# Kernel optimization log

Hardware: AMD Instinct MI355X
Metric: run time of the kernel (lower is better)

## Reference

```python
import jax, jax.numpy as jnp
import numpy as np

HEADS = 8
EPS = 1e-5


def _layernorm(x, g, b):
    mu = jnp.mean(x, axis=-1, keepdims=True)
    var = jnp.mean(jnp.square(x - mu), axis=-1, keepdims=True)
    return (x - mu) * jax.lax.rsqrt(var + EPS) * g + b


def setup_inputs() -> dict:
    key = jax.random.key(0)
    ks = jax.random.split(key, 10)
    B, S, D = 4, 2048, 256
    d_ff = 2 * D
    s = 0.02
    return {
        "x": jax.random.normal(ks[0], (B, S, D), dtype=jnp.float32),
        "ln1_g": jnp.ones((D,), jnp.float32),
        "ln1_b": jnp.zeros((D,), jnp.float32),
        "w_qkv": jax.random.normal(ks[1], (3 * D, D), jnp.float32) * s,
        "b_qkv": jnp.zeros((3 * D,), jnp.float32),
        "w_proj": jax.random.normal(ks[2], (D, D), jnp.float32) * s,
        "b_proj": jnp.zeros((D,), jnp.float32),
        "ln2_g": jnp.ones((D,), jnp.float32),
        "ln2_b": jnp.zeros((D,), jnp.float32),
        "w1": jax.random.normal(ks[3], (d_ff, D), jnp.float32) * s,
        "b1": jnp.zeros((d_ff,), jnp.float32),
        "w2": jax.random.normal(ks[4], (D, d_ff), jnp.float32) * s,
        "b2": jnp.zeros((D,), jnp.float32),
    }


def reference(x, ln1_g, ln1_b, w_qkv, b_qkv, w_proj, b_proj,
              ln2_g, ln2_b, w1, b1, w2, b2):
    B, S, D = x.shape
    H = HEADS
    dh = D // H
    scale = dh ** -0.5

    # --- attention sublayer (pre-LN) ---
    y = _layernorm(x, ln1_g, ln1_b)
    qkv = y @ w_qkv.T + b_qkv                       # [B,S,3D]
    qkv = qkv.reshape(B, S, 3, H, dh)
    q = jnp.transpose(qkv[:, :, 0], (0, 2, 1, 3))   # [B,H,S,dh]
    k = jnp.transpose(qkv[:, :, 1], (0, 2, 1, 3))
    v = jnp.transpose(qkv[:, :, 2], (0, 2, 1, 3))
    attn = jax.nn.softmax(jnp.einsum('bhsd,bhtd->bhst', q, k) * scale, axis=-1)
    ctx = jnp.einsum('bhst,bhtd->bhsd', attn, v)    # [B,H,S,dh]
    ctx = jnp.transpose(ctx, (0, 2, 1, 3)).reshape(B, S, D)
    x = x + ctx @ w_proj.T + b_proj

    # --- FFN sublayer (pre-LN) ---
    y = _layernorm(x, ln2_g, ln2_b)
    h = jax.nn.silu(y @ w1.T + b1)                  # [B,S,2D]
    x = x + h @ w2.T + b2
    return x
```

## Files before the change

### kernel.cpp

```cpp
#include <hip/hip_runtime.h>
#include <cstddef>

constexpr int kB   = 4;
constexpr int kS   = 2048;
constexpr int kD   = 256;
constexpr int kH   = 8;
constexpr int kDH  = 32;
constexpr int kDFF = 512;
constexpr int kM   = kB * kS;
constexpr float kEps = 1e-5f;
constexpr float kScaleL2E = 0.17677669529663687f * 1.4426950408889634f;

typedef float f32x4  __attribute__((ext_vector_type(4)));
typedef short bf16x8 __attribute__((ext_vector_type(8)));
typedef unsigned short u16;
typedef unsigned int   u32;

__device__ inline u16 f2bf(float x) {
    union { float f; unsigned u; } c; c.f = x;
    const unsigned r = c.u + 0x7fffu + ((c.u >> 16) & 1u);
    return (u16)(r >> 16);
}

__device__ inline u32 pk_trunc(float lo, float hi) {
    union { float f; u32 u; } a, b; a.f = lo; b.f = hi;
    return __builtin_amdgcn_perm(b.u, a.u, 0x07060302u);
}

__global__ __launch_bounds__(256)
void ln_kernel(const float* __restrict__ x, const float* __restrict__ g,
               const float* __restrict__ b, u16* __restrict__ y)
{
    const int wave = threadIdx.x >> 6;
    const int lane = threadIdx.x & 63;
    const int row  = blockIdx.x * 4 + wave;
    const float4 v = *(const float4*)&x[(size_t)row * kD + lane * 4];
    float s1 = (v.x + v.y) + (v.z + v.w);
    float s2 = (v.x * v.x + v.y * v.y) + (v.z * v.z + v.w * v.w);
    #pragma unroll
    for (int off = 1; off < 64; off <<= 1) {
        s1 += __shfl_xor(s1, off);
        s2 += __shfl_xor(s2, off);
    }
    const float mu  = s1 * (1.0f / kD);
    const float var = s2 * (1.0f / kD) - mu * mu;
    const float inv = rsqrtf(var + kEps);
    const float4 g4 = *(const float4*)&g[lane * 4];
    const float4 b4 = *(const float4*)&b[lane * 4];
    *(ushort4*)&y[(size_t)row * kD + lane * 4] = make_ushort4(
        f2bf((v.x - mu) * inv * g4.x + b4.x),
        f2bf((v.y - mu) * inv * g4.y + b4.y),
        f2bf((v.z - mu) * inv * g4.z + b4.z),
        f2bf((v.w - mu) * inv * g4.w + b4.w));
}

template<int NT, int OUTMODE, bool RES, int KTOT, int MLOOP>
__global__ __launch_bounds__(256)
void gemm_bf16(const u16* __restrict__ A, const float* __restrict__ Wf,
               const float* __restrict__ bias, const float* __restrict__ res,
               float* __restrict__ Cf, u16* __restrict__ Cb,
               u16* __restrict__ KbP, u16* __restrict__ VtP, int N)
{
    constexpr int BSTR = KTOT + 4;
    __shared__ u16 Bs[NT * BSTR];
    const int tid  = threadIdx.x;
    const int wave = tid >> 6;
    const int lane = tid & 63;
    const int quad = lane >> 4;
    const int l16  = lane & 15;
    const int mbase = blockIdx.x * (64 * MLOOP);
    const int n0 = blockIdx.y * NT;

    {
        constexpr int ITS = (NT * KTOT) / 1024;
        #pragma unroll
        for (int it = 0; it < ITS; ++it) {
            const int e   = it * 1024 + tid * 4;
            const int row = e / KTOT;
            const int col = e & (KTOT - 1);
            const float4 wv = *(const float4*)&Wf[(size_t)(n0 + row) * KTOT + col];
            *(ushort4*)&Bs[row * BSTR + col] = make_ushort4(
                f2bf(wv.x), f2bf(wv.y), f2bf(wv.z), f2bf(wv.w));
        }
    }
    __syncthreads();

    #pragma unroll 1
    for (int mi = 0; mi < MLOOP; ++mi) {
        const int m0 = mbase + mi * 64;

        f32x4 acc[NT / 16];
        #pragma unroll
        for (int ni = 0; ni < NT / 16; ++ni) acc[ni] = {0.f, 0.f, 0.f, 0.f};

        const u16* arow = &A[(size_t)(m0 + wave * 16 + l16) * KTOT];
        #pragma unroll 4
        for (int k0 = 0; k0 < KTOT; k0 += 32) {
            const bf16x8 a = *(const bf16x8*)&arow[k0 + quad * 8];
            #pragma unroll
            for (int ni = 0; ni < NT / 16; ++ni) {
                const bf16x8 bf = *(const bf16x8*)&Bs[(ni * 16 + l16) * BSTR + k0 + quad * 8];
                acc[ni] = __builtin_amdgcn_mfma_f32_16x16x32_bf16(a, bf, acc[ni], 0, 0, 0);
            }
        }

        #pragma unroll
        for (int ni = 0; ni < NT / 16; ++ni) {
            const float bias_v = bias[n0 + ni * 16 + l16];
            #pragma unroll
            for (int r = 0; r < 4; ++r) {
                const int m = m0 + wave * 16 + quad * 4 + r;
                float v = acc[ni][r] + bias_v;
                if (OUTMODE == 0) {
                    const int n = n0 + ni * 16 + l16;
                    if (RES) v += res[(size_t)m * N + n];
                    Cf[(size_t)m * N + n] = v;
                } else if (OUTMODE == 1) {
                    const int n = n0 + ni * 16 + l16;
                    v = v / (1.0f + __expf(-v));
                    Cb[(size_t)m * N + n] = f2bf(v);
                } else {
                    const int rgn = n0 >> 8;
                    const int nl  = (n0 & 255) + ni * 16 + l16;
                    const int hh  = nl >> 5, dh = nl & 31;
                    const int bb  = m >> 11, s = m & (kS - 1);
                    const int bh  = bb * kH + hh;
                    if (rgn == 0)
                        Cb[((size_t)bh * kS + s) * kDH + dh] = f2bf(v * kScaleL2E);
                    else if (rgn == 1)
                        KbP[((size_t)bh * kS + s) * kDH + dh] = f2bf(v);
                    else {
                        const int sp = (s & ~63) | (((s & 15) << 2) | ((s >> 4) & 3));
                        VtP[(((size_t)bh * (kS / 8) + (sp >> 3)) * kDH + dh) * 8 + (sp & 7)] = f2bf(v);
                    }
                }
            }
        }
    }
}

constexpr int kPStrU = 72;

__global__ __launch_bounds__(256)
void attn_kernel(const u16* __restrict__ Qb, const u16* __restrict__ Kb,
                 const u16* __restrict__ Vp, u16* __restrict__ ctx)
{
    __shared__ __align__(16) u16 pbuf[4][32 * kPStrU];
    const int tid  = threadIdx.x;
    const int wave = tid >> 6;
    const int lane = tid & 63;
    const int quad = lane >> 4;
    const int l16  = lane & 15;
    const int h = blockIdx.y;
    const int b = blockIdx.z;
    const int bh = b * kH + h;
    const int q0 = blockIdx.x * 32;

    bf16x8 aq[2];
    aq[0] = *(const bf16x8*)&Qb[((size_t)bh * kS + q0 + l16) * kDH + quad * 8];
    aq[1] = *(const bf16x8*)&Qb[((size_t)bh * kS + q0 + 16 + l16) * kDH + quad * 8];

    const u16* Kbase = Kb + (size_t)bh * kS * kDH;
    const u16* Vbase = Vp + (size_t)bh * kS * kDH;
    u16* pw = pbuf[wave];

    f32x4 O[2][2] = {};
    f32x4 lp[2] = {};
    const f32x4 zz = {0.f, 0.f, 0.f, 0.f};

    const int kbeg = wave * (kS / 4);
    #pragma unroll 1
    for (int kt = kbeg; kt < kbeg + kS / 4; kt += 64) {
        bf16x8 kf[4];
        #pragma unroll
        for (int kg = 0; kg < 4; ++kg)
            kf[kg] = *(const bf16x8*)
                &Kbase[(size_t)(kt + kg * 16 + l16) * kDH + quad * 8];
        bf16x8 vf[2][2];
        #pragma unroll
        for (int ks = 0; ks < 2; ++ks)
            #pragma unroll
            for (int nf = 0; nf < 2; ++nf)
                vf[ks][nf] = *(const bf16x8*)
                    &Vbase[(size_t)((((kt + ks * 32 + quad * 8) >> 3) * kDH
                                     + nf * 16 + l16) << 3)];

        #pragma unroll
        for (int qb = 0; qb < 2; ++qb) {
            f32x4 S[4];
            #pragma unroll
            for (int kg = 0; kg < 4; ++kg)
                S[kg] = __builtin_amdgcn_mfma_f32_16x16x32_bf16(aq[qb], kf[kg], zz, 0, 0, 0);
            #pragma unroll
            for (int r = 0; r < 4; ++r) {
                const float e0 = exp2f(S[0][r]);
                const float e1 = exp2f(S[1][r]);
                const float e2 = exp2f(S[2][r]);
                const float e3 = exp2f(S[3][r]);
                lp[qb][r] += (e0 + e1) + (e2 + e3);
                uint2 pk;
                pk.x = pk_trunc(e0, e1);
                pk.y = pk_trunc(e2, e3);
                *(uint2*)&pw[(qb * 16 + quad * 4 + r) * kPStrU + l16 * 4] = pk;
            }
        }

        #pragma unroll
        for (int qb = 0; qb < 2; ++qb)
            #pragma unroll
            for (int ks = 0; ks < 2; ++ks) {
                const bf16x8 pA = *(const bf16x8*)
                    &pw[(qb * 16 + l16) * kPStrU + ks * 32 + quad * 8];
                O[qb][0] = __builtin_amdgcn_mfma_f32_16x16x32_bf16(pA, vf[ks][0], O[qb][0], 0, 0, 0);
                O[qb][1] = __builtin_amdgcn_mfma_f32_16x16x32_bf16(pA, vf[ks][1], O[qb][1], 0, 0, 0);
            }
    }

    #pragma unroll
    for (int off = 1; off < 16; off <<= 1)
        #pragma unroll
        for (int qb = 0; qb < 2; ++qb)
            #pragma unroll
            for (int r = 0; r < 4; ++r)
                lp[qb][r] += __shfl_xor(lp[qb][r], off);

    __syncthreads();
    float* cbase = (float*)&pbuf[0][0];
    if (wave > 0) {
        float* cb = cbase + (wave - 1) * (32 * 33);
        #pragma unroll
        for (int qb = 0; qb < 2; ++qb)
            #pragma unroll
            for (int r = 0; r < 4; ++r) {
                const int row = qb * 16 + quad * 4 + r;
                cb[row * 33 + l16]      = O[qb][0][r];
                cb[row * 33 + 16 + l16] = O[qb][1][r];
                if (l16 == 0) cb[row * 33 + 32] = lp[qb][r];
            }
    }
    __syncthreads();
    if (wave == 0) {
        #pragma unroll
        for (int qb = 0; qb < 2; ++qb)
            #pragma unroll
            for (int r = 0; r < 4; ++r) {
                const int row = qb * 16 + quad * 4 + r;
                float l  = lp[qb][r];
                float o0 = O[qb][0][r];
                float o1 = O[qb][1][r];
                #pragma unroll
                for (int s = 0; s < 3; ++s) {
                    const float* cb = cbase + s * (32 * 33);
                    o0 += cb[row * 33 + l16];
                    o1 += cb[row * 33 + 16 + l16];
                    l  += cb[row * 33 + 32];
                }
                const float inv = 1.0f / l;
                const int q = q0 + row;
                u16* crow = ctx + ((size_t)(b * kS + q)) * kD + h * kDH;
                crow[l16]      = f2bf(o0 * inv);
                crow[16 + l16] = f2bf(o1 * inv);
            }
    }
}

extern "C" void kernel_launch(void* const* d_in, const int* in_sizes, int n_in,
                              void* d_out, int out_size, void* d_ws, size_t ws_size,
                              hipStream_t stream)
{
    const float* x      = (const float*)d_in[0];
    const float* ln1_g  = (const float*)d_in[1];
    const float* ln1_b  = (const float*)d_in[2];
    const float* w_qkv  = (const float*)d_in[3];
    const float* b_qkv  = (const float*)d_in[4];
    const float* w_proj = (const float*)d_in[5];
    const float* b_proj = (const float*)d_in[6];
    const float* ln2_g  = (const float*)d_in[7];
    const float* ln2_b  = (const float*)d_in[8];
    const float* w1     = (const float*)d_in[9];
    const float* b1     = (const float*)d_in[10];
    const float* w2     = (const float*)d_in[11];
    const float* b2     = (const float*)d_in[12];
    float* out = (float*)d_out;

    char* ws = (char*)d_ws;
    u16* Qb  = (u16*)ws;
    u16* Kb  = (u16*)(ws + ((size_t)4  << 20));
    u16* Vp  = (u16*)(ws + ((size_t)8  << 20));
    u16* ctx = (u16*)(ws + ((size_t)12 << 20));
    u16* y   = (u16*)(ws + ((size_t)16 << 20));
    u16* h   = (u16*)ws;

    const dim3 blk(256);

    ln_kernel<<<dim3(kM / 4), blk, 0, stream>>>(x, ln1_g, ln1_b, y);
    gemm_bf16<64, 2, false, 256, 2><<<dim3(kM / 128, 12), blk, 0, stream>>>(
        y, w_qkv, b_qkv, nullptr, nullptr, Qb, Kb, Vp, 0);
    attn_kernel<<<dim3(kS / 32, kH, kB), blk, 0, stream>>>(Qb, Kb, Vp, ctx);
    gemm_bf16<32, 0, true, 256, 2><<<dim3(kM / 128, kD / 32), blk, 0, stream>>>(
        ctx, w_proj, b_proj, x, out, nullptr, nullptr, nullptr, kD);
    ln_kernel<<<dim3(kM / 4), blk, 0, stream>>>(out, ln2_g, ln2_b, y);
    gemm_bf16<64, 1, false, 256, 2><<<dim3(kM / 128, kDFF / 64), blk, 0, stream>>>(
        y, w1, b1, nullptr, nullptr, h, nullptr, nullptr, kDFF);
    gemm_bf16<32, 0, true, 512, 2><<<dim3(kM / 128, kD / 32), blk, 0, stream>>>(
        h, w2, b2, out, out, nullptr, nullptr, nullptr, kD);
}
```

Measured before the change: 184.6 us.

## Split attention waves across two query tiles and enlarge GEMM row tiles

The attention kernel now gives each block 64 queries, with two waves per 32-query tile each covering half the keys, instead of four waves splitting the keys for one 32-query tile. Blocks use a flat 1024-entry grid with an interleaved batch-head mapping, and the cross-wave reduction becomes a single pairwise merge. This halves the number of attention blocks and cuts LDS reduction traffic, at the cost of longer per-wave key loops. Separately, every GEMM switches its last template parameter from 2 to 4 and halves the row-block grid, so each block covers 256 rows and can reuse weights more, with fewer blocks left to fill the GPU.

```diff
diff --git a/kernel.cpp b/kernel.cpp
--- a/kernel.cpp
+++ b/kernel.cpp
@@ -151,10 +151,13 @@
     const int lane = tid & 63;
     const int quad = lane >> 4;
     const int l16  = lane & 15;
-    const int h = blockIdx.y;
-    const int b = blockIdx.z;
-    const int bh = b * kH + h;
-    const int q0 = blockIdx.x * 32;
+    const int n    = blockIdx.x;
+    const int bh   = (n & 7) * 4 + ((n >> 3) & 3);
+    const int b    = bh >> 3;
+    const int h    = bh & 7;
+    const int qsub = wave >> 1;
+    const int half = wave & 1;
+    const int q0 = (n >> 5) * 64 + qsub * 32;
 
     bf16x8 aq[2];
     aq[0] = *(const bf16x8*)&Qb[((size_t)bh * kS + q0 + l16) * kDH + quad * 8];
@@ -168,9 +171,9 @@
     f32x4 lp[2] = {};
     const f32x4 zz = {0.f, 0.f, 0.f, 0.f};
 
-    const int kbeg = wave * (kS / 4);
+    const int kbeg = half * (kS / 2);
     #pragma unroll 1
-    for (int kt = kbeg; kt < kbeg + kS / 4; kt += 64) {
+    for (int kt = kbeg; kt < kbeg + kS / 2; kt += 64) {
         bf16x8 kf[4];
         #pragma unroll
         for (int kg = 0; kg < 4; ++kg)
@@ -225,9 +228,8 @@
                 lp[qb][r] += __shfl_xor(lp[qb][r], off);
 
     __syncthreads();
-    float* cbase = (float*)&pbuf[0][0];
-    if (wave > 0) {
-        float* cb = cbase + (wave - 1) * (32 * 33);
+    float* cb = (float*)&pbuf[0][0] + qsub * (32 * 33);
+    if (half == 1) {
         #pragma unroll
         for (int qb = 0; qb < 2; ++qb)
             #pragma unroll
@@ -239,23 +241,16 @@
             }
     }
     __syncthreads();
-    if (wave == 0) {
+    if (half == 0) {
         #pragma unroll
         for (int qb = 0; qb < 2; ++qb)
             #pragma unroll
             for (int r = 0; r < 4; ++r) {
                 const int row = qb * 16 + quad * 4 + r;
-                float l  = lp[qb][r];
-                float o0 = O[qb][0][r];
-                float o1 = O[qb][1][r];
-                #pragma unroll
-                for (int s = 0; s < 3; ++s) {
-                    const float* cb = cbase + s * (32 * 33);
-                    o0 += cb[row * 33 + l16];
-                    o1 += cb[row * 33 + 16 + l16];
-                    l  += cb[row * 33 + 32];
-                }
+                const float l   = lp[qb][r] + cb[row * 33 + 32];
                 const float inv = 1.0f / l;
+                const float o0 = O[qb][0][r] + cb[row * 33 + l16];
+                const float o1 = O[qb][1][r] + cb[row * 33 + 16 + l16];
                 const int q = q0 + row;
                 u16* crow = ctx + ((size_t)(b * kS + q)) * kD + h * kDH;
                 crow[l16]      = f2bf(o0 * inv);
@@ -294,14 +289,14 @@
     const dim3 blk(256);
 
     ln_kernel<<<dim3(kM / 4), blk, 0, stream>>>(x, ln1_g, ln1_b, y);
-    gemm_bf16<64, 2, false, 256, 2><<<dim3(kM / 128, 12), blk, 0, stream>>>(
+    gemm_bf16<64, 2, false, 256, 4><<<dim3(kM / 256, 12), blk, 0, stream>>>(
         y, w_qkv, b_qkv, nullptr, nullptr, Qb, Kb, Vp, 0);
-    attn_kernel<<<dim3(kS / 32, kH, kB), blk, 0, stream>>>(Qb, Kb, Vp, ctx);
-    gemm_bf16<32, 0, true, 256, 2><<<dim3(kM / 128, kD / 32), blk, 0, stream>>>(
+    attn_kernel<<<dim3(1024), blk, 0, stream>>>(Qb, Kb, Vp, ctx);
+    gemm_bf16<32, 0, true, 256, 4><<<dim3(kM / 256, kD / 32), blk, 0, stream>>>(
         ctx, w_proj, b_proj, x, out, nullptr, nullptr, nullptr, kD);
     ln_kernel<<<dim3(kM / 4), blk, 0, stream>>>(out, ln2_g, ln2_b, y);
-    gemm_bf16<64, 1, false, 256, 2><<<dim3(kM / 128, kDFF / 64), blk, 0, stream>>>(
+    gemm_bf16<64, 1, false, 256, 4><<<dim3(kM / 256, kDFF / 64), blk, 0, stream>>>(
         y, w1, b1, nullptr, nullptr, h, nullptr, nullptr, kDFF);
-    gemm_bf16<32, 0, true, 512, 2><<<dim3(kM / 128, kD / 32), blk, 0, stream>>>(
+    gemm_bf16<32, 0, true, 512, 4><<<dim3(kM / 256, kD / 32), blk, 0, stream>>>(
         h, w2, b2, out, out, nullptr, nullptr, nullptr, kD);
 }
```

New measurement: 195.9 us. 6.1% more time.
